# Optimization experiments

Hardware: AMD Instinct MI355X
Metric: run time of the kernel (lower is better)

The kernel has to match this reference:

```python
import jax, jax.numpy as jnp
from jax import lax
import numpy as np

B, C, H, W = 32, 128, 64, 64
OUT, KH, KW = 128, 3, 3
E, INTERM = 4, 256


def setup_inputs() -> dict:
    key = jax.random.key(0)
    k1, k2, k3, k4 = jax.random.split(key, 4)
    x = jax.random.normal(k1, (B, C, H, W), dtype=jnp.float32)
    routing_w = jax.random.normal(k2, (INTERM, C), dtype=jnp.float32) * 0.05
    routing_b = jax.random.normal(k3, (INTERM,), dtype=jnp.float32) * 0.05
    expert_weight = jax.random.normal(k4, (E, OUT * C * KH * KW), dtype=jnp.float32) * 0.05
    return {"x": x, "routing_w": routing_w, "routing_b": routing_b, "expert_weight": expert_weight}


def reference(x, routing_w, routing_b, expert_weight):
    b = x.shape[0]
    # adaptive_avg_pool2d(x, 1).flatten(1)
    pooled = x.mean(axis=(2, 3))                              # [B, C]
    rt = jax.nn.sigmoid(pooled @ routing_w.T + routing_b)     # [B, 256]
    # avg_pool1d kernel=stride=interm_d//num_experts
    routing = rt.reshape(b, E, INTERM // E).mean(axis=-1)     # [B, E]
    # CondConv2d: per-sample mixed kernels, grouped conv over batch
    w = routing @ expert_weight                               # [B, OUT*C*KH*KW]
    w = w.reshape(b * OUT, C, KH, KW)                         # OIHW, O grouped by sample
    xg = x.reshape(1, b * C, H, W)
    y = lax.conv_general_dilated(
        xg, w,
        window_strides=(1, 1),
        padding=((1, 1), (1, 1)),
        dimension_numbers=('NCHW', 'OIHW', 'NCHW'),
        feature_group_count=b,
    )
    return y.reshape(b, OUT, H, W)
```

## Files before the change

### kernel.cpp

```cpp
#include <hip/hip_runtime.h>

typedef __attribute__((ext_vector_type(8))) short short8;
typedef __attribute__((ext_vector_type(4))) short shortv4;
typedef __attribute__((ext_vector_type(4))) float f32x4;

#define B_      32
#define C_      128
#define H_      64
#define W_      64
#define OUT_    128
#define PLANE   4096
#define EWSZ    147456

__device__ inline short f2bf(float f) {
    unsigned u = __builtin_bit_cast(unsigned, f);
    u += 0x7fff + ((u >> 16) & 1);
    return (short)(u >> 16);
}

__global__ void pool_kernel(const float* __restrict__ x, float* __restrict__ pooled) {
    const int bc = blockIdx.x;
    const float4* plane = (const float4*)(x + (size_t)bc * PLANE);
    float s = 0.f;
#pragma unroll
    for (int i = 0; i < 4; ++i) {
        float4 v = plane[threadIdx.x + i * 256];
        s += v.x + v.y + v.z + v.w;
    }
#pragma unroll
    for (int off = 32; off > 0; off >>= 1) s += __shfl_down(s, off);
    __shared__ float ls[4];
    const int wave = threadIdx.x >> 6, lane = threadIdx.x & 63;
    if (lane == 0) ls[wave] = s;
    __syncthreads();
    if (threadIdx.x == 0)
        pooled[bc] = (ls[0] + ls[1] + ls[2] + ls[3]) * (1.f / 4096.f);
}

__global__ void routing_kernel(const float* __restrict__ pooled,
                               const float* __restrict__ rw,
                               const float* __restrict__ rb,
                               float* __restrict__ routing) {
    const int b = blockIdx.x;
    __shared__ float ps[C_];
    if (threadIdx.x < C_) ps[threadIdx.x] = pooled[b * C_ + threadIdx.x];
    __syncthreads();
    const int i = threadIdx.x;
    const float4* w4 = (const float4*)(rw + (size_t)i * C_);
    float z = rb[i];
#pragma unroll 8
    for (int c4 = 0; c4 < 32; ++c4) {
        float4 wv = w4[c4];
        z += wv.x * ps[c4 * 4 + 0] + wv.y * ps[c4 * 4 + 1]
           + wv.z * ps[c4 * 4 + 2] + wv.w * ps[c4 * 4 + 3];
    }
    float s = 1.f / (1.f + expf(-z));
#pragma unroll
    for (int off = 32; off > 0; off >>= 1) s += __shfl_down(s, off);
    if ((threadIdx.x & 63) == 0)
        routing[b * 4 + (threadIdx.x >> 6)] = s * (1.f / 64.f);
}

__global__ void epack_kernel(const float* __restrict__ ew, float* __restrict__ epk) {
    const int os = blockIdx.x;
    const int cc = blockIdx.y;
    const int e  = blockIdx.z;
    __shared__ float ls[16 * 292];
    const int tid = threadIdx.x;

    for (int idx = tid; idx < 1152; idx += 256) {
        const int i = idx / 72, q = idx % 72;
        float4 v = *(const float4*)(ew + (size_t)e * EWSZ
                     + (size_t)(os * 16 + i) * 1152 + cc * 288 + q * 4);
        *(float4*)&ls[i * 292 + q * 4] = v;
    }
    __syncthreads();

    float* outp = epk + ((size_t)e * 4 + cc) * 36864;
    for (int idx = tid; idx < 1152; idx += 256) {
        const int t = idx / 128, r = idx % 128;
        const int l = r >> 1, j0 = (r & 1) * 4;
        const int row = l & 15, cb = (l >> 4) * 8 + j0;
        float4 v;
        v.x = ls[row * 292 + (cb + 0) * 9 + t];
        v.y = ls[row * 292 + (cb + 1) * 9 + t];
        v.z = ls[row * 292 + (cb + 2) * 9 + t];
        v.w = ls[row * 292 + (cb + 3) * 9 + t];
        *(float4*)(outp + (size_t)(t * 8 + os) * 512 + r * 4) = v;
    }
}

__global__ void wmix_kernel(const float* __restrict__ rbuf,
                            const float* __restrict__ epk,
                            short* __restrict__ wbuf) {
#pragma unroll
    for (int it = 0; it < 2; ++it) {
        const int idx = blockIdx.x * 512 + it * 256 + threadIdx.x;
        const int b = idx / 36864;
        const int r = idx - b * 36864;
        const float r0 = rbuf[b * 4 + 0], r1 = rbuf[b * 4 + 1];
        const float r2 = rbuf[b * 4 + 2], r3 = rbuf[b * 4 + 3];
        float4 a = *(const float4*)(epk + (size_t)r * 4);
        float4 bb = *(const float4*)(epk + 147456 + (size_t)r * 4);
        float4 c = *(const float4*)(epk + 2 * 147456 + (size_t)r * 4);
        float4 d = *(const float4*)(epk + 3 * 147456 + (size_t)r * 4);
        shortv4 v;
        v[0] = f2bf(r0 * a.x + r1 * bb.x + r2 * c.x + r3 * d.x);
        v[1] = f2bf(r0 * a.y + r1 * bb.y + r2 * c.y + r3 * d.y);
        v[2] = f2bf(r0 * a.z + r1 * bb.z + r2 * c.z + r3 * d.z);
        v[3] = f2bf(r0 * a.w + r1 * bb.w + r2 * c.w + r3 * d.w);
        *(shortv4*)(wbuf + (size_t)b * 147456 + (size_t)r * 4) = v;
    }
}

__global__ __launch_bounds__(256, 2) void conv_kernel(const float* __restrict__ x,
                                                      const short* __restrict__ wbuf,
                                                      float* __restrict__ out) {
    __shared__ __attribute__((aligned(16))) short xs_s[15840];
    __shared__ __attribute__((aligned(16))) short ws_s[20480];

    const int b = blockIdx.x, hb = blockIdx.y;
    const int h0 = hb * 4;
    const int tid = threadIdx.x;
    const int wid = tid >> 6, lane = tid & 63;
    const int ln15 = lane & 15, lg = lane >> 4;

    for (int i = tid; i < 7920; i += 256) ((int*)xs_s)[i] = 0;

    f32x4 acc[8][4];
#pragma unroll
    for (int m = 0; m < 8; ++m)
#pragma unroll
        for (int n = 0; n < 4; ++n) acc[m][n] = (f32x4){0.f, 0.f, 0.f, 0.f};

    const float* xb = x + (size_t)b * C_ * PLANE;
    const short* wsrc_b = wbuf + (size_t)b * 4 * 36864;

    int tw[6], tr[6], tcg[6], trow[6];
#pragma unroll
    for (int it = 0; it < 6; ++it) {
        const int task = it * 256 + tid;
        tw[it] = task & 63;
        const int rc = task >> 6;
        tr[it] = rc % 6;
        tcg[it] = rc / 6;
        trow[it] = h0 - 1 + tr[it];
    }

    short8 xpre[6];
#define LOADX(CCC)                                                              \
    {                                                                           \
        _Pragma("unroll")                                                       \
        for (int it = 0; it < 6; ++it) {                                        \
            const bool valid = (unsigned)trow[it] < 64u;                        \
            const float* src = xb + (size_t)((CCC) * 32 + tcg[it] * 8) * PLANE  \
                             + trow[it] * 64 + tw[it];                          \
            short8 v;                                                           \
            _Pragma("unroll")                                                   \
            for (int k = 0; k < 8; ++k)                                         \
                v[k] = f2bf(valid ? src[(size_t)k * PLANE] : 0.f);              \
            xpre[it] = v;                                                       \
        }                                                                       \
    }

#define DO_TAP(TL, T)                                                           \
    {                                                                           \
        const int kh = (T) / 3, kw = (T) % 3;                                   \
        short8 bfr[4];                                                          \
        _Pragma("unroll")                                                       \
        for (int nf = 0; nf < 4; ++nf)                                          \
            bfr[nf] = *(const short8*)&xs_s[((wid + kh) * 66 + nf * 16 + ln15 + kw) * 40 + lg * 8]; \
        _Pragma("unroll")                                                       \
        for (int mf = 0; mf < 8; ++mf) {                                        \
            short8 af = *(const short8*)&ws_s[(((TL) * 8 + mf) * 64 + lane) * 8]; \
            _Pragma("unroll")                                                   \
            for (int nf = 0; nf < 4; ++nf)                                      \
                acc[mf][nf] = __builtin_amdgcn_mfma_f32_16x16x32_bf16(          \
                    af, bfr[nf], acc[mf][nf], 0, 0, 0);                         \
        }                                                                       \
    }

    LOADX(0);
    __syncthreads();

    for (int cc = 0; cc < 4; ++cc) {
#pragma unroll
        for (int it = 0; it < 6; ++it)
            *(short8*)&xs_s[((tr[it] * 66) + 1 + tw[it]) * 40 + tcg[it] * 8] = xpre[it];

        const char* srcb = (const char*)(wsrc_b + (size_t)cc * 36864);
#pragma unroll
        for (int it = 0; it < 8; ++it) {
            const int off = (wid * 8 + it) * 1024 + lane * 16;
            __builtin_amdgcn_global_load_lds(
                (const __attribute__((address_space(1))) void*)(srcb + off),
                (__attribute__((address_space(3))) void*)(((char*)ws_s) + off), 16, 0, 0);
        }
        __syncthreads();

        DO_TAP(0, 0) DO_TAP(1, 1) DO_TAP(2, 2) DO_TAP(3, 3)
        __syncthreads();

#pragma unroll
        for (int it = 0; it < 10; ++it) {
            const int off = (wid * 10 + it) * 1024 + lane * 16;
            __builtin_amdgcn_global_load_lds(
                (const __attribute__((address_space(1))) void*)(srcb + 32768 + off),
                (__attribute__((address_space(3))) void*)(((char*)ws_s) + off), 16, 0, 0);
        }
        __syncthreads();

        if (cc < 3) LOADX(cc + 1);

        DO_TAP(0, 4) DO_TAP(1, 5) DO_TAP(2, 6) DO_TAP(3, 7) DO_TAP(4, 8)
        __syncthreads();
    }

    float* ob = out + (size_t)b * OUT_ * PLANE;
    const int h = h0 + wid;
#pragma unroll
    for (int mf = 0; mf < 8; ++mf) {
#pragma unroll
        for (int nf = 0; nf < 4; ++nf) {
            const int w = nf * 16 + ln15;
            const int o0 = mf * 16 + lg * 4;
#pragma unroll
            for (int q = 0; q < 4; ++q)
                ob[((size_t)(o0 + q) * 64 + h) * 64 + w] = acc[mf][nf][q];
        }
    }
#undef LOADX
#undef DO_TAP
}

extern "C" void kernel_launch(void* const* d_in, const int* in_sizes, int n_in,
                              void* d_out, int out_size, void* d_ws, size_t ws_size,
                              hipStream_t stream) {
    const float* x  = (const float*)d_in[0];
    const float* rw = (const float*)d_in[1];
    const float* rb = (const float*)d_in[2];
    const float* ew = (const float*)d_in[3];
    float* out = (float*)d_out;

    float* pooled  = (float*)d_ws;
    float* routing = pooled + 4096;
    float* epk     = pooled + 8192;
    short* wbuf    = (short*)(epk + 589824);

    epack_kernel<<<dim3(8, 4, 4), 256, 0, stream>>>(ew, epk);
    pool_kernel<<<dim3(B_ * C_), 256, 0, stream>>>(x, pooled);
    routing_kernel<<<dim3(B_), 256, 0, stream>>>(pooled, rw, rb, routing);
    wmix_kernel<<<dim3(2304), 256, 0, stream>>>(routing, epk, wbuf);
    conv_kernel<<<dim3(B_, 16), 256, 0, stream>>>(x, wbuf, out);
}
```

Measured before the change: 197.9 us.

## Double-buffer conv weight staging, widen blocks to 8 rows with 512 threads

The conv kernel now uses 512-thread blocks covering 8 output rows each, halving the grid and sharing each weight tile across twice as many rows. Weight taps are staged in three-tap parts into two ping-pong LDS buffers, so the next part loads while the current one feeds the MFMAs. The x loads for the next channel chunk are issued as raw fp32 early and converted later. MFMA sections are wrapped in setprio and sched_barrier. LDS use per block grows to about 100KB, which may limit occupancy, and there are still several syncs per chunk.

```diff
diff --git a/kernel.cpp b/kernel.cpp
--- a/kernel.cpp
+++ b/kernel.cpp
@@ -113,19 +113,19 @@
     }
 }
 
-__global__ __launch_bounds__(256, 2) void conv_kernel(const float* __restrict__ x,
+__global__ __launch_bounds__(512, 2) void conv_kernel(const float* __restrict__ x,
                                                       const short* __restrict__ wbuf,
                                                       float* __restrict__ out) {
-    __shared__ __attribute__((aligned(16))) short xs_s[15840];
-    __shared__ __attribute__((aligned(16))) short ws_s[20480];
+    __shared__ __attribute__((aligned(16))) short xs_s[26400];
+    __shared__ __attribute__((aligned(16))) short ws_s[2][12288];
 
     const int b = blockIdx.x, hb = blockIdx.y;
-    const int h0 = hb * 4;
+    const int h0 = hb * 8;
     const int tid = threadIdx.x;
     const int wid = tid >> 6, lane = tid & 63;
     const int ln15 = lane & 15, lg = lane >> 4;
 
-    for (int i = tid; i < 7920; i += 256) ((int*)xs_s)[i] = 0;
+    for (int i = tid; i < 13200; i += 512) ((int*)xs_s)[i] = 0;
 
     f32x4 acc[8][4];
 #pragma unroll
@@ -134,36 +134,57 @@
         for (int n = 0; n < 4; ++n) acc[m][n] = (f32x4){0.f, 0.f, 0.f, 0.f};
 
     const float* xb = x + (size_t)b * C_ * PLANE;
-    const short* wsrc_b = wbuf + (size_t)b * 4 * 36864;
-
-    int tw[6], tr[6], tcg[6], trow[6];
-#pragma unroll
-    for (int it = 0; it < 6; ++it) {
-        const int task = it * 256 + tid;
+    const char* wsrc_b = (const char*)(wbuf + (size_t)b * 4 * 36864);
+
+    int tw[5], tr[5], tcg[5];
+    bool tvalid[5];
+    const float* tsrc[5];
+#pragma unroll
+    for (int it = 0; it < 5; ++it) {
+        const int task = it * 512 + tid;
         tw[it] = task & 63;
         const int rc = task >> 6;
-        tr[it] = rc % 6;
-        tcg[it] = rc / 6;
-        trow[it] = h0 - 1 + tr[it];
-    }
-
-    short8 xpre[6];
-#define LOADX(CCC)                                                              \
-    {                                                                           \
-        _Pragma("unroll")                                                       \
-        for (int it = 0; it < 6; ++it) {                                        \
-            const bool valid = (unsigned)trow[it] < 64u;                        \
-            const float* src = xb + (size_t)((CCC) * 32 + tcg[it] * 8) * PLANE  \
-                             + trow[it] * 64 + tw[it];                          \
+        tr[it] = rc % 10;
+        tcg[it] = rc / 10;
+        const int trow = h0 - 1 + tr[it];
+        tvalid[it] = (unsigned)trow < 64u;
+        const int rowc = trow < 0 ? 0 : (trow > 63 ? 63 : trow);
+        tsrc[it] = xb + (size_t)(tcg[it] * 8) * PLANE + rowc * 64 + tw[it];
+    }
+
+    float xraw[5][8];
+#define LOADX(CC)                                                               \
+    {                                                                           \
+        _Pragma("unroll")                                                       \
+        for (int it = 0; it < 5; ++it)                                          \
+            _Pragma("unroll")                                                   \
+            for (int k = 0; k < 8; ++k)                                         \
+                xraw[it][k] = tsrc[it][(size_t)((CC) * 32 + k) * PLANE];        \
+    }
+#define WRITE_XS()                                                              \
+    {                                                                           \
+        _Pragma("unroll")                                                       \
+        for (int it = 0; it < 5; ++it) {                                        \
             short8 v;                                                           \
             _Pragma("unroll")                                                   \
             for (int k = 0; k < 8; ++k)                                         \
-                v[k] = f2bf(valid ? src[(size_t)k * PLANE] : 0.f);              \
-            xpre[it] = v;                                                       \
+                v[k] = tvalid[it] ? f2bf(xraw[it][k]) : (short)0;               \
+            *(short8*)&xs_s[((tr[it] * 66) + 1 + tw[it]) * 40 + tcg[it] * 8] = v; \
         }                                                                       \
     }
-
-#define DO_TAP(TL, T)                                                           \
+#define STAGE(BUF, CC, PART)                                                    \
+    {                                                                           \
+        const char* srcp = wsrc_b + (CC) * 73728 + (PART) * 24576;              \
+        char* dstp = (char*)(&ws_s[BUF][0]);                                    \
+        _Pragma("unroll")                                                       \
+        for (int it = 0; it < 3; ++it) {                                        \
+            const int off = (wid * 3 + it) * 1024 + lane * 16;                  \
+            __builtin_amdgcn_global_load_lds(                                   \
+                (const __attribute__((address_space(1))) void*)(srcp + off),    \
+                (__attribute__((address_space(3))) void*)(dstp + off), 16, 0, 0); \
+        }                                                                       \
+    }
+#define DO_TAP(BUF, TL, T)                                                      \
     {                                                                           \
         const int kh = (T) / 3, kw = (T) % 3;                                   \
         short8 bfr[4];                                                          \
@@ -172,49 +193,47 @@
             bfr[nf] = *(const short8*)&xs_s[((wid + kh) * 66 + nf * 16 + ln15 + kw) * 40 + lg * 8]; \
         _Pragma("unroll")                                                       \
         for (int mf = 0; mf < 8; ++mf) {                                        \
-            short8 af = *(const short8*)&ws_s[(((TL) * 8 + mf) * 64 + lane) * 8]; \
+            short8 af = *(const short8*)&ws_s[BUF][(((TL) * 8 + mf) * 64 + lane) * 8]; \
             _Pragma("unroll")                                                   \
             for (int nf = 0; nf < 4; ++nf)                                      \
                 acc[mf][nf] = __builtin_amdgcn_mfma_f32_16x16x32_bf16(          \
                     af, bfr[nf], acc[mf][nf], 0, 0, 0);                         \
         }                                                                       \
     }
+#define DO_PART(BUF, T0)                                                        \
+    __builtin_amdgcn_s_setprio(1);                                              \
+    DO_TAP(BUF, 0, (T0) + 0) DO_TAP(BUF, 1, (T0) + 1) DO_TAP(BUF, 2, (T0) + 2) \
+    __builtin_amdgcn_s_setprio(0);
 
     LOADX(0);
-    __syncthreads();
-
-    for (int cc = 0; cc < 4; ++cc) {
-#pragma unroll
-        for (int it = 0; it < 6; ++it)
-            *(short8*)&xs_s[((tr[it] * 66) + 1 + tw[it]) * 40 + tcg[it] * 8] = xpre[it];
-
-        const char* srcb = (const char*)(wsrc_b + (size_t)cc * 36864);
-#pragma unroll
-        for (int it = 0; it < 8; ++it) {
-            const int off = (wid * 8 + it) * 1024 + lane * 16;
-            __builtin_amdgcn_global_load_lds(
-                (const __attribute__((address_space(1))) void*)(srcb + off),
-                (__attribute__((address_space(3))) void*)(((char*)ws_s) + off), 16, 0, 0);
-        }
-        __syncthreads();
-
-        DO_TAP(0, 0) DO_TAP(1, 1) DO_TAP(2, 2) DO_TAP(3, 3)
-        __syncthreads();
-
-#pragma unroll
-        for (int it = 0; it < 10; ++it) {
-            const int off = (wid * 10 + it) * 1024 + lane * 16;
-            __builtin_amdgcn_global_load_lds(
-                (const __attribute__((address_space(1))) void*)(srcb + 32768 + off),
-                (__attribute__((address_space(3))) void*)(((char*)ws_s) + off), 16, 0, 0);
-        }
-        __syncthreads();
-
-        if (cc < 3) LOADX(cc + 1);
-
-        DO_TAP(0, 4) DO_TAP(1, 5) DO_TAP(2, 6) DO_TAP(3, 7) DO_TAP(4, 8)
-        __syncthreads();
-    }
+    STAGE(0, 0, 0);
+    __syncthreads();
+    WRITE_XS();
+    STAGE(1, 0, 1);
+    __syncthreads();
+
+#define CHUNK(CC, BA, BB)                                                       \
+    DO_PART(BA, 0)                                         \
+    __syncthreads();                                                            \
+    STAGE(BA, CC, 2);                                       \
+    if ((CC) < 3) LOADX((CC) + 1);                                              \
+    __builtin_amdgcn_sched_barrier(0);                                          \
+    DO_PART(BB, 3)                                         \
+    __syncthreads();                                                            \
+    if ((CC) < 3) STAGE(BB, (CC) + 1, 0);                 \
+    __builtin_amdgcn_sched_barrier(0);                                          \
+    DO_PART(BA, 6)                                         \
+    __syncthreads();                                                            \
+    if ((CC) < 3) {                                                             \
+        WRITE_XS();                                                             \
+        STAGE(BA, (CC) + 1, 1);                           \
+        __syncthreads();                                                        \
+    }
+
+    CHUNK(0, 0, 1)
+    CHUNK(1, 1, 0)
+    CHUNK(2, 0, 1)
+    CHUNK(3, 1, 0)
 
     float* ob = out + (size_t)b * OUT_ * PLANE;
     const int h = h0 + wid;
@@ -230,7 +249,11 @@
         }
     }
 #undef LOADX
+#undef WRITE_XS
+#undef STAGE
 #undef DO_TAP
+#undef DO_PART
+#undef CHUNK
 }
 
 extern "C" void kernel_launch(void* const* d_in, const int* in_sizes, int n_in,
@@ -251,5 +274,5 @@
     pool_kernel<<<dim3(B_ * C_), 256, 0, stream>>>(x, pooled);
     routing_kernel<<<dim3(B_), 256, 0, stream>>>(pooled, rw, rb, routing);
     wmix_kernel<<<dim3(2304), 256, 0, stream>>>(routing, epk, wbuf);
-    conv_kernel<<<dim3(B_, 16), 256, 0, stream>>>(x, wbuf, out);
-}
+    conv_kernel<<<dim3(B_, 8), 512, 0, stream>>>(x, wbuf, out);
+}
```

Result: faster. 166.5 us (-15.9%).
